# Optimization experiments

Hardware: AMD Instinct MI355X
Metric: run time of the kernel (lower is better)

Reference implementation:

```python
import jax, jax.numpy as jnp
import numpy as np

N_NODES = 100000
N_EDGES = 1600000
N_GRAPHS = 256
F_IN = 54


def setup_inputs() -> dict:
    key = jax.random.key(0)
    ks = jax.random.split(key, 16)
    x = jax.random.normal(ks[0], (N_NODES, F_IN), dtype=jnp.float32)
    edge_index = jax.random.randint(ks[1], (2, N_EDGES), 0, N_NODES, dtype=jnp.int32)
    batch = jnp.sort(jax.random.randint(ks[2], (N_NODES,), 0, N_GRAPHS, dtype=jnp.int32))

    def lin(k, fi, fo):
        kw, kb = jax.random.split(k)
        lim = 1.0 / np.sqrt(fi)
        W = jax.random.uniform(kw, (fi, fo), minval=-lim, maxval=lim, dtype=jnp.float32)
        b = jax.random.uniform(kb, (fo,), minval=-lim, maxval=lim, dtype=jnp.float32)
        return W, b

    W1, b1 = lin(ks[3], 54, 54)
    W2, b2 = lin(ks[4], 54, 108)
    W3, b3 = lin(ks[5], 108, 216)
    Wf1, bf1 = lin(ks[6], 216, 1024)
    Wf2, bf2 = lin(ks[7], 1024, 128)
    return {"x": x, "edge_index": edge_index, "batch": batch,
            "W1": W1, "b1": b1, "W2": W2, "b2": b2, "W3": W3, "b3": b3,
            "Wf1": Wf1, "bf1": bf1, "Wf2": Wf2, "bf2": bf2}


def _gcn_norm(edge_index, n):
    # add self-loops, symmetric degree normalization (PyG GCNConv default)
    loop = jnp.arange(n, dtype=edge_index.dtype)
    row = jnp.concatenate([edge_index[0], loop])
    col = jnp.concatenate([edge_index[1], loop])
    deg = jax.ops.segment_sum(jnp.ones_like(col, dtype=jnp.float32), col, num_segments=n)
    dinv = jnp.where(deg > 0, jax.lax.rsqrt(deg), 0.0)
    norm = dinv[row] * dinv[col]
    return row, col, norm


def _gcn_conv(x, row, col, norm, W, b, n):
    h = x @ W                                  # [N, Fout]
    msg = h[row] * norm[:, None]               # [E+N, Fout] gather + scale
    out = jax.ops.segment_sum(msg, col, num_segments=n)  # scatter-add
    return out + b


def reference(x, edge_index, batch, W1, b1, W2, b2, W3, b3, Wf1, bf1, Wf2, bf2):
    n = x.shape[0]
    row, col, norm = _gcn_norm(edge_index, n)
    h = jax.nn.relu(_gcn_conv(x, row, col, norm, W1, b1, n))
    h = jax.nn.relu(_gcn_conv(h, row, col, norm, W2, b2, n))
    h = jax.nn.relu(_gcn_conv(h, row, col, norm, W3, b3, n))
    # global mean pool per graph
    sums = jax.ops.segment_sum(h, batch, num_segments=N_GRAPHS)
    cnts = jax.ops.segment_sum(jnp.ones((n,), jnp.float32), batch, num_segments=N_GRAPHS)
    pooled = sums / jnp.maximum(cnts, 1.0)[:, None]   # [G, 216]
    g = jax.nn.relu(pooled @ Wf1 + bf1)               # dropout = identity (eval)
    return g @ Wf2 + bf2                              # [G, 128]
```

## Files before the change

### kernel.cpp

```cpp
#include <hip/hip_runtime.h>


typedef _Float16 f16;
typedef _Float16 f16x2 __attribute__((ext_vector_type(2)));
typedef _Float16 f16x8 __attribute__((ext_vector_type(8)));
typedef float f32x4 __attribute__((ext_vector_type(4)));

static __host__ __device__ inline int cdiv(int a, int b) { return (a + b - 1) / b; }

constexpr int BSPAN = 512;
constexpr int EPB   = 4096;
constexpr int EPT   = EPB / 256;

__device__ __forceinline__ void wpack_one(const float* W, f16* Wb, int K, int F,
                                          int KT, int idx) {
    int j = idx & 7;
    int lane = (idx >> 3) & 63;
    int fi = idx >> 9;
    int kt = fi % KT;
    int nt = fi / KT;
    int k = kt * 32 + (lane >> 4) * 8 + j;
    int nn = nt * 16 + (lane & 15);
    Wb[idx] = (k < K && nn < F) ? (f16)W[k * F + nn] : (f16)0.f;
}

__global__ __launch_bounds__(256) void k_init(
        const int* __restrict__ batch, int* __restrict__ start,
        float* __restrict__ psum, int* __restrict__ bktCnt, int* __restrict__ bktCur,
        const int* __restrict__ col,
        const float* __restrict__ W1, const float* __restrict__ W2,
        const float* __restrict__ W3, f16* __restrict__ w1b,
        f16* __restrict__ w2b, f16* __restrict__ w3b,
        int e, int nb, int n, int g) {
    __shared__ int hist[256];
    int t = threadIdx.x;
    int i = blockIdx.x * blockDim.x + t;
    hist[t] = 0;
    __syncthreads();
    int ebase = blockIdx.x * EPB;
#pragma unroll
    for (int j = 0; j < EPT; j++) {
        int idx = ebase + j * 256 + t;
        if (idx < e) atomicAdd(&hist[col[idx] >> 9], 1);
    }
    if (i < g * 216) psum[i] = 0.f;
    if (i < 256) bktCur[i] = 0;
    constexpr int T1 = 4 * 2 * 512;
    constexpr int T2 = 7 * 2 * 512;
    constexpr int T3 = 14 * 4 * 512;
    if (i < T1) wpack_one(W1, w1b, 54, 54, 2, i);
    else if (i < T1 + T2) wpack_one(W2, w2b, 54, 108, 2, i - T1);
    else if (i < T1 + T2 + T3) wpack_one(W3, w3b, 108, 216, 4, i - T1 - T2);
    if (i < n) {
        int b = batch[i];
        int bp = (i == 0) ? -1 : batch[i - 1];
        for (int gg = bp + 1; gg <= b; gg++) start[gg] = i;
        if (i == n - 1)
            for (int gg = b + 1; gg <= g; gg++) start[gg] = n;
    }
    __syncthreads();
    if (t < nb && hist[t] > 0) atomicAdd(&bktCnt[t], hist[t]);
}

__device__ __forceinline__ int scan256_ex(int* sbuf, int v, int t) {
    sbuf[t] = v;
    __syncthreads();
    for (int off = 1; off < 256; off <<= 1) {
        int x = sbuf[t];
        int y = (t >= off) ? sbuf[t - off] : 0;
        __syncthreads();
        sbuf[t] = x + y;
        __syncthreads();
    }
    return sbuf[t] - v;
}

__global__ __launch_bounds__(256) void k_bkt_part(const int* __restrict__ row,
                                                  const int* __restrict__ col,
                                                  const int* __restrict__ bktCnt,
                                                  int* bktCur, unsigned int* __restrict__ ebuf,
                                                  int e, int nb) {
    __shared__ int sbuf[256];
    __shared__ int hist[256];
    __shared__ int base[256];
    __shared__ int lcur[256];
    int t = threadIdx.x;
    int boff = scan256_ex(sbuf, (t < nb) ? bktCnt[t] : 0, t);
    hist[t] = 0; lcur[t] = 0;
    __syncthreads();
    int bs = blockIdx.x * EPB;
    unsigned int pk[EPT];
    int b[EPT];
#pragma unroll
    for (int j = 0; j < EPT; j++) {
        int idx = bs + j * 256 + t;
        if (idx < e) {
            int c = col[idx];
            pk[j] = ((unsigned int)(c & (BSPAN - 1)) << 17) | (unsigned int)row[idx];
            b[j] = c >> 9;
            atomicAdd(&hist[b[j]], 1);
        } else b[j] = -1;
    }
    __syncthreads();
    if (t < nb && hist[t] > 0) base[t] = boff + atomicAdd(&bktCur[t], hist[t]);
    __syncthreads();
#pragma unroll
    for (int j = 0; j < EPT; j++) {
        if (b[j] >= 0) {
            int lofs = atomicAdd(&lcur[b[j]], 1);
            ebuf[base[b[j]] + lofs] = pk[j];
        }
    }
}

__global__ __launch_bounds__(256) void k_bkt_build(const unsigned int* __restrict__ ebuf,
                                                   const int* __restrict__ bktCnt,
                                                   int* __restrict__ rowptr,
                                                   float* __restrict__ dinv,
                                                   int* __restrict__ eSrc,
                                                   int n, int nb) {
    __shared__ int sbuf[256];
    __shared__ int hist[BSPAN];
    __shared__ int cur[BSPAN];
    int t = threadIdx.x;
    int bkt = blockIdx.x;

    int boff_ex = scan256_ex(sbuf, (t < nb) ? bktCnt[t] : 0, t);
    __shared__ int boff_s, cnt_s;
    if (t == bkt) boff_s = boff_ex;
    if (t == 0) cnt_s = bktCnt[bkt];
    hist[t] = 0; hist[t + 256] = 0;
    __syncthreads();
    int es = boff_s, ee = boff_s + cnt_s;

    {
        int i = es + t;
        for (; i + 3 * 256 < ee; i += 4 * 256) {
            unsigned p0 = ebuf[i], p1 = ebuf[i + 256], p2 = ebuf[i + 512], p3 = ebuf[i + 768];
            atomicAdd(&hist[p0 >> 17], 1);
            atomicAdd(&hist[p1 >> 17], 1);
            atomicAdd(&hist[p2 >> 17], 1);
            atomicAdd(&hist[p3 >> 17], 1);
        }
        for (; i < ee; i += 256) atomicAdd(&hist[ebuf[i] >> 17], 1);
    }
    __syncthreads();

    int h0 = hist[2 * t], h1 = hist[2 * t + 1];
    __syncthreads();
    int ex = scan256_ex(sbuf, h0 + h1, t);
    int e0 = es + ex, e1 = e0 + h0;

    int node0 = bkt * BSPAN;
    int n0 = node0 + 2 * t, n1 = node0 + 2 * t + 1;
    if (n0 <= n) rowptr[n0] = e0;
    if (n1 <= n) rowptr[n1] = e1;
    if (n0 < n) dinv[n0] = rsqrtf((float)(h0 + 1));
    if (n1 < n) dinv[n1] = rsqrtf((float)(h1 + 1));
    cur[2 * t] = e0; cur[2 * t + 1] = e1;
    __syncthreads();

    {
        int i = es + t;
        for (; i + 3 * 256 < ee; i += 4 * 256) {
            unsigned p0 = ebuf[i], p1 = ebuf[i + 256], p2 = ebuf[i + 512], p3 = ebuf[i + 768];
            int s0 = atomicAdd(&cur[p0 >> 17], 1);
            int s1 = atomicAdd(&cur[p1 >> 17], 1);
            int s2 = atomicAdd(&cur[p2 >> 17], 1);
            int s3 = atomicAdd(&cur[p3 >> 17], 1);
            eSrc[s0] = (int)(p0 & 0x1FFFFu);
            eSrc[s1] = (int)(p1 & 0x1FFFFu);
            eSrc[s2] = (int)(p2 & 0x1FFFFu);
            eSrc[s3] = (int)(p3 & 0x1FFFFu);
        }
        for (; i < ee; i += 256) {
            unsigned int p = ebuf[i];
            int slot = atomicAdd(&cur[p >> 17], 1);
            eSrc[slot] = (int)(p & 0x1FFFFu);
        }
    }
}

template <int F, int RS>
__global__ void k_prescale(const float* __restrict__ x, const float* __restrict__ dinv,
                           f16* __restrict__ xs, int n) {
    constexpr int CH = F / 2;
    int idx = blockIdx.x * blockDim.x + threadIdx.x;
    if (idx >= n * CH) return;
    int node = idx / CH;
    int c = idx - node * CH;
    float d = dinv[node];
    float2 v = *reinterpret_cast<const float2*>(x + (long long)node * F + c * 2);
    f16x2 h;
    h[0] = (f16)(v.x * d);
    h[1] = (f16)(v.y * d);
    *reinterpret_cast<f16x2*>(xs + (long long)node * RS + c * 2) = h;
}

template <int F, int RS>
__global__ __launch_bounds__(256) void k_gatherw(
        const int* __restrict__ rowptr, const int* __restrict__ eSrc,
        const float* __restrict__ dinv, const f16* __restrict__ hs,
        f16* __restrict__ out, int n) {
    constexpr int CGN = RS / 8;
    constexpr int EPW = 64 / CGN;
    int wave = threadIdx.x >> 6;
    int lane = threadIdx.x & 63;
    int eslot = lane / CGN;
    int cg = lane & (CGN - 1);
    int node = blockIdx.x * 4 + wave;
    if (node >= n) return;
    int ch0 = cg * 8;
    int lim = F - ch0;
    if (lim > 8) lim = 8;
    if (lim < 0) lim = 0;

    int rs_ = rowptr[node], re = rowptr[node + 1];
    float di = dinv[node];
    int deg = re - rs_;
    int myidx = 0;
    if (lane < deg) myidx = eSrc[rs_ + lane];

    const f16x8* src = reinterpret_cast<const f16x8*>(hs);
    float acc[8];
#pragma unroll
    for (int j = 0; j < 8; j++) acc[j] = 0.f;

    if (eslot == 0) {
        f16x8 v = src[(long long)node * CGN + cg];
#pragma unroll
        for (int j = 0; j < 8; j++) acc[j] += (float)v[j];
    }

    int nfull = deg < 64 ? deg : 64;
    for (int base = 0; base < nfull; base += 8 * EPW) {
        int sidx[8];
#pragma unroll
        for (int u = 0; u < 8; u++) {
            int idx = base + u * EPW + eslot;
            sidx[u] = __shfl(myidx, idx < 63 ? idx : 63);
        }
        f16x8 v[8];
#pragma unroll
        for (int u = 0; u < 8; u++) {
            int idx = base + u * EPW + eslot;
            if (idx < nfull) v[u] = src[(long long)sidx[u] * CGN + cg];
        }
#pragma unroll
        for (int u = 0; u < 8; u++) {
            int idx = base + u * EPW + eslot;
            if (idx < nfull) {
#pragma unroll
                for (int j = 0; j < 8; j++) acc[j] += (float)v[u][j];
            }
        }
    }
    for (int e = rs_ + 64 + eslot; e < re; e += EPW) {
        int s = eSrc[e];
        f16x8 v = src[(long long)s * CGN + cg];
#pragma unroll
        for (int j = 0; j < 8; j++) acc[j] += (float)v[j];
    }

#pragma unroll
    for (int j = 0; j < 8; j++)
        if (j >= lim) acc[j] = 0.f;
#pragma unroll
    for (int m = CGN; m < 64; m <<= 1)
#pragma unroll
        for (int j = 0; j < 8; j++) acc[j] += __shfl_xor(acc[j], m);

    if (eslot == 0) {
        f16x8 o;
#pragma unroll
        for (int j = 0; j < 8; j++) o[j] = (f16)(acc[j] * di);
        *reinterpret_cast<f16x8*>(out + (long long)node * RS + ch0) = o;
    }
}

template <int F, int KTILES, int NTILES, int FOUT, int OSTR>
__global__ __launch_bounds__(256) void k_gcn_fused(
        const int* __restrict__ rowptr, const int* __restrict__ eSrc,
        const float* __restrict__ dinv, const f16* __restrict__ hs,
        const f16* __restrict__ Wb, const float* __restrict__ bias,
        f16* __restrict__ outh, int n) {
    constexpr int KPAD = KTILES * 32;
    constexpr int KP   = KPAD + 8;
    constexpr int CGN  = KPAD / 8;
    constexpr int EPH  = 32 / CGN;

    __shared__ __align__(16) f16 a_lds[64 * KP];

    int t = threadIdx.x;
    int node0 = blockIdx.x * 64;
    int w = t >> 6;
    int lane = t & 63;
    int half = lane >> 5;
    int l = lane & 31;
    int eslot = l / CGN;
    int cg = l & (CGN - 1);
    int ch0 = cg * 8;
    int lim = F - ch0;
    if (lim > 8) lim = 8;
    if (lim < 0) lim = 0;
    int lbase = half * 32;

    const f16x8* src = reinterpret_cast<const f16x8*>(hs);
    int nodeBase = node0 + w * 16;

    for (int i = 0; i < 8; i++) {
        int node = nodeBase + 2 * i + half;
        float acc[8];
#pragma unroll
        for (int j = 0; j < 8; j++) acc[j] = 0.f;
        float di = 0.f;

        if (node < n) {
            int rs_ = rowptr[node], re = rowptr[node + 1];
            di = dinv[node];
            int deg = re - rs_;
            int myidx = 0;
            if (l < deg) myidx = eSrc[rs_ + l];

            if (eslot == 0) {
                f16x8 v = src[(long long)node * CGN + cg];
#pragma unroll
                for (int j = 0; j < 8; j++) acc[j] += (float)v[j];
            }

            int nfull = deg < 32 ? deg : 32;
            if (nfull > 0) {
                int sidx[8];
#pragma unroll
                for (int u = 0; u < 8; u++) {
                    int idx = u * EPH + eslot;
                    sidx[u] = __shfl(myidx, lbase + (idx < 31 ? idx : 31));
                }
                f16x8 v[8];
#pragma unroll
                for (int u = 0; u < 8; u++) {
                    int idx = u * EPH + eslot;
                    if (idx < nfull) v[u] = src[(long long)sidx[u] * CGN + cg];
                }
#pragma unroll
                for (int u = 0; u < 8; u++) {
                    int idx = u * EPH + eslot;
                    if (idx < nfull) {
#pragma unroll
                        for (int j = 0; j < 8; j++) acc[j] += (float)v[u][j];
                    }
                }
            }
            for (int e = rs_ + 32 + eslot; e < re; e += EPH) {
                int s = eSrc[e];
                f16x8 v = src[(long long)s * CGN + cg];
#pragma unroll
                for (int j = 0; j < 8; j++) acc[j] += (float)v[j];
            }

#pragma unroll
            for (int j = 0; j < 8; j++)
                if (j >= lim) acc[j] = 0.f;
#pragma unroll
            for (int m = CGN; m < 32; m <<= 1)
#pragma unroll
                for (int j = 0; j < 8; j++) acc[j] += __shfl_xor(acc[j], m);
        }

        if (eslot == 0) {
            f16x8 o;
#pragma unroll
            for (int j = 0; j < 8; j++) o[j] = (f16)(acc[j] * di);
            *reinterpret_cast<f16x8*>(&a_lds[(w * 16 + 2 * i + half) * KP + ch0]) = o;
        }
    }
    __syncthreads();

    int quad = lane >> 4;
    int col = lane & 15;

    f16x8 afr[KTILES];
#pragma unroll
    for (int kt = 0; kt < KTILES; kt++)
        afr[kt] = *reinterpret_cast<const f16x8*>(
            &a_lds[(16 * w + col) * KP + kt * 32 + quad * 8]);

    int nodeC = node0 + 16 * w + quad * 4;
    float dv[4];
#pragma unroll
    for (int r = 0; r < 4; r++) {
        int nd = nodeC + r;
        dv[r] = (nd < n) ? dinv[nd] : 0.f;
    }

    const f16x8* wb = reinterpret_cast<const f16x8*>(Wb);
#pragma unroll
    for (int nt = 0; nt < NTILES; nt++) {
        f16x8 bfr[KTILES];
#pragma unroll
        for (int kt = 0; kt < KTILES; kt++)
            bfr[kt] = wb[(nt * KTILES + kt) * 64 + lane];
        f32x4 acc = {0.f, 0.f, 0.f, 0.f};
#pragma unroll
        for (int kt = 0; kt < KTILES; kt++)
            acc = __builtin_amdgcn_mfma_f32_16x16x32_f16(afr[kt], bfr[kt], acc, 0, 0, 0);

        int ch = nt * 16 + col;
        if (ch < FOUT) {
            float bval = bias[ch];
#pragma unroll
            for (int r = 0; r < 4; r++) {
                int nd = nodeC + r;
                if (nd < n)
                    outh[(long long)nd * OSTR + ch] =
                        (f16)(fmaxf(acc[r] + bval, 0.f) * dv[r]);
            }
        }
    }
}

template <int KTILES, int NTILES, int K, int FOUT>
__global__ __launch_bounds__(256) void k_gemm_pool(
        const f16* __restrict__ in, const f16* __restrict__ Wb,
        const float* __restrict__ bias, const int* __restrict__ batch,
        float* __restrict__ psum, int n) {
    constexpr int KPAD = KTILES * 32;
    constexpr int KP   = KPAD + 8;
    constexpr int V8   = KPAD / 8;
    constexpr int NSLOT = 4;

    __shared__ f16 a_lds[64 * KP];
    __shared__ float psum_l[NSLOT * FOUT];

    int t = threadIdx.x;
    int node0 = blockIdx.x * 64;

    const f16x8* inp = reinterpret_cast<const f16x8*>(in);
    for (int f = t; f < 64 * V8; f += 256) {
        int node = f / V8;
        int v = f - node * V8;
        f16x8 val = {};
        if (node0 + node < n) val = inp[(long long)(node0 + node) * V8 + v];
        *reinterpret_cast<f16x8*>(&a_lds[node * KP + v * 8]) = val;
    }
    for (int i = t; i < NSLOT * FOUT; i += 256) psum_l[i] = 0.f;
    __syncthreads();

    int w = t >> 6;
    int lane = t & 63;
    int quad = lane >> 4;
    int col = lane & 15;

    f16x8 afr[KTILES];
#pragma unroll
    for (int kt = 0; kt < KTILES; kt++)
        afr[kt] = *reinterpret_cast<const f16x8*>(
            &a_lds[(16 * w + col) * KP + kt * 32 + quad * 8]);

    int nodeC = node0 + 16 * w + quad * 4;
    int gb[4];
#pragma unroll
    for (int r = 0; r < 4; r++) {
        int nd = nodeC + r;
        gb[r] = (nd < n) ? batch[nd] : -1;
    }
    int g0 = batch[node0];

    const f16x8* wb = reinterpret_cast<const f16x8*>(Wb);
#pragma unroll
    for (int nt = 0; nt < NTILES; nt++) {
        f16x8 bfr[KTILES];
#pragma unroll
        for (int kt = 0; kt < KTILES; kt++)
            bfr[kt] = wb[(nt * KTILES + kt) * 64 + lane];
        f32x4 acc = {0.f, 0.f, 0.f, 0.f};
#pragma unroll
        for (int kt = 0; kt < KTILES; kt++)
            acc = __builtin_amdgcn_mfma_f32_16x16x32_f16(afr[kt], bfr[kt], acc, 0, 0, 0);

        int ch = nt * 16 + col;
        if (ch < FOUT) {
            float bval = bias[ch];
            if (gb[0] == gb[3] && gb[0] >= 0) {
                float s = fmaxf(acc[0] + bval, 0.f) + fmaxf(acc[1] + bval, 0.f)
                        + fmaxf(acc[2] + bval, 0.f) + fmaxf(acc[3] + bval, 0.f);
                int slot = gb[0] - g0;
                if (slot < NSLOT) atomicAdd(&psum_l[slot * FOUT + ch], s);
                else atomicAdd(&psum[gb[0] * FOUT + ch], s);
            } else {
#pragma unroll
                for (int r = 0; r < 4; r++) {
                    if (gb[r] < 0) continue;
                    float v = fmaxf(acc[r] + bval, 0.f);
                    int slot = gb[r] - g0;
                    if (slot < NSLOT) atomicAdd(&psum_l[slot * FOUT + ch], v);
                    else atomicAdd(&psum[gb[r] * FOUT + ch], v);
                }
            }
        }
    }

    __syncthreads();
    int lastNode = node0 + 63;
    if (lastNode >= n) lastNode = n - 1;
    int nsl = batch[lastNode] - g0 + 1;
    if (nsl > NSLOT) nsl = NSLOT;
    for (int f = t; f < nsl * FOUT; f += 256) {
        float v = psum_l[f];
        if (v != 0.f) atomicAdd(&psum[(g0 + f / FOUT) * FOUT + (f % FOUT)], v);
    }
}

__global__ void k_fc1(const float* __restrict__ P, const int* __restrict__ start,
                      const float* __restrict__ W, const float* __restrict__ bias,
                      float* __restrict__ out) {
    int row = blockIdx.x >> 2;
    int o = (blockIdx.x & 3) * 256 + threadIdx.x;
    int cnt = start[row + 1] - start[row];
    float scale = 1.0f / fmaxf((float)cnt, 1.0f);
    __shared__ float prow[216];
    if (threadIdx.x < 216) prow[threadIdx.x] = P[row * 216 + threadIdx.x] * scale;
    __syncthreads();
    float acc = bias[o];
    for (int k = 0; k < 216; k++) acc += prow[k] * W[k * 1024 + o];
    out[row * 1024 + o] = fmaxf(acc, 0.f);
}
__global__ void k_fc2(const float* __restrict__ G, const float* __restrict__ W,
                      const float* __restrict__ bias, float* __restrict__ out) {
    int row = blockIdx.x;
    int o = threadIdx.x;
    __shared__ float grow[1024];
    for (int k = threadIdx.x; k < 1024; k += 128) grow[k] = G[row * 1024 + k];
    __syncthreads();
    float acc = bias[o];
    for (int k = 0; k < 1024; k++) acc += grow[k] * W[k * 128 + o];
    out[row * 128 + o] = acc;
}

extern "C" void kernel_launch(void* const* d_in, const int* in_sizes, int n_in,
                              void* d_out, int out_size, void* d_ws, size_t ws_size,
                              hipStream_t stream) {
    const float* x     = (const float*)d_in[0];
    const int*   ei    = (const int*)d_in[1];
    const int*   batch = (const int*)d_in[2];
    const float* W1  = (const float*)d_in[3];
    const float* b1  = (const float*)d_in[4];
    const float* W2  = (const float*)d_in[5];
    const float* b2  = (const float*)d_in[6];
    const float* W3  = (const float*)d_in[7];
    const float* b3  = (const float*)d_in[8];
    const float* Wf1 = (const float*)d_in[9];
    const float* bf1 = (const float*)d_in[10];
    const float* Wf2 = (const float*)d_in[11];
    const float* bf2 = (const float*)d_in[12];
    float* out = (float*)d_out;

    const int N = in_sizes[0] / 54;
    const int E = in_sizes[1] / 2;
    const int G = 256;
    const int* row = ei;
    const int* col = ei + E;
    const int NB = cdiv(N, BSPAN);
    const int NBLK_A = cdiv(E, EPB);

    char* ws = (char*)d_ws;
    size_t off = 0;
    auto carve = [&](size_t bytes) {
        void* p = ws + off;
        off += (bytes + 255) & ~(size_t)255;
        return p;
    };
    int*   rowptr  = (int*)carve((size_t)(N + 1) * 4);
    int*   bktCnt  = (int*)carve(256 * 4);
    int*   bktCur  = (int*)carve(256 * 4);
    int*   eSrc    = (int*)carve((size_t)E * 4);
    float* dinv    = (float*)carve((size_t)N * 4);
    f16*   xs      = (f16*)carve((size_t)N * 64 * 2);
    f16*   hsbuf   = (f16*)carve((size_t)N * 128 * 2);
    f16*   bufA    = (f16*)carve((size_t)N * 128 * 2);
    unsigned int* ebuf = (unsigned int*)carve((size_t)E * 4);
    float* psum    = (float*)carve((size_t)G * 216 * 4);
    float* gbuf    = (float*)carve((size_t)G * 1024 * 4);
    int*   start   = (int*)carve((size_t)(G + 1) * 4);
    f16*   w1b     = (f16*)carve((size_t)4 * 2 * 512 * 2);
    f16*   w2b     = (f16*)carve((size_t)7 * 2 * 512 * 2);
    f16*   w3b     = (f16*)carve((size_t)14 * 4 * 512 * 2);

    const int T = 256;
    hipMemsetAsync(bktCnt, 0, 256 * 4, stream);

    int gInit = cdiv(N, T) > NBLK_A ? cdiv(N, T) : NBLK_A;
    k_init<<<gInit, T, 0, stream>>>(batch, start, psum, bktCnt, bktCur, col,
                                    W1, W2, W3, w1b, w2b, w3b, E, NB, N, G);

    k_bkt_part<<<NBLK_A, 256, 0, stream>>>(row, col, bktCnt, bktCur, ebuf, E, NB);
    k_bkt_build<<<NB, 256, 0, stream>>>(ebuf, bktCnt, rowptr, dinv, eSrc, N, NB);

    k_prescale<54, 64><<<cdiv(N * 27, T), T, 0, stream>>>(x, dinv, xs, N);

    const int GB = cdiv(N, 64);

    k_gcn_fused<54, 2, 4, 54, 64><<<GB, 256, 0, stream>>>(
        rowptr, eSrc, dinv, xs, w1b, b1, hsbuf, N);

    k_gcn_fused<54, 2, 7, 108, 128><<<GB, 256, 0, stream>>>(
        rowptr, eSrc, dinv, hsbuf, w2b, b2, bufA, N);

    k_gatherw<108, 128><<<cdiv(N, 4), 256, 0, stream>>>(rowptr, eSrc, dinv, bufA, hsbuf, N);
    k_gemm_pool<4, 14, 108, 216><<<GB, 256, 0, stream>>>(
        hsbuf, w3b, b3, batch, psum, N);

    k_fc1<<<G * 4, T, 0, stream>>>(psum, start, Wf1, bf1, gbuf);
    k_fc2<<<G, 128, 0, stream>>>(gbuf, Wf2, bf2, out);
}
```

Measured before the change: 379.6 us.

## Prefetch next node's row pointers and neighbor indices in GCN aggregation loop

Loads all 17 rowptr entries and 16 dinv values for the warp's nodes once up front and distributes them by shuffle, replacing per-node scalar loads. Software-pipelines the per-node loop so the next node's edge-index load and self-feature load are issued while the current node's neighbor gathers are in flight. This hides the dependent rowptr->eSrc->feature latency chain, at the cost of extra registers that may lower occupancy.

```diff
diff --git a/kernel.cpp b/kernel.cpp
--- a/kernel.cpp
+++ b/kernel.cpp
@@ -308,71 +308,89 @@
     const f16x8* src = reinterpret_cast<const f16x8*>(hs);
     int nodeBase = node0 + w * 16;
 
+    int rpIdx = nodeBase + (lane < 17 ? lane : 16);
+    if (rpIdx > n) rpIdx = n;
+    int rp = rowptr[rpIdx];
+    int dvIdx = nodeBase + (lane < 16 ? lane : 15);
+    if (dvIdx > n - 1) dvIdx = n - 1;
+    float dvl = dinv[dvIdx];
+
+    int rs_c = __shfl(rp, half);
+    int re_c = __shfl(rp, 1 + half);
+    int deg_c = re_c - rs_c;
+    int my_c = 0;
+    if (l < deg_c) my_c = eSrc[rs_c + l];
+    f16x8 sv_c = {};
+    if (eslot == 0 && nodeBase + half < n)
+        sv_c = src[(long long)(nodeBase + half) * CGN + cg];
+
     for (int i = 0; i < 8; i++) {
         int node = nodeBase + 2 * i + half;
+        int nfull = deg_c < 32 ? deg_c : 32;
+
+        int sidx[8];
+#pragma unroll
+        for (int u = 0; u < 8; u++) {
+            int idx = u * EPH + eslot;
+            sidx[u] = __shfl(my_c, lbase + (idx < 31 ? idx : 31));
+        }
+        f16x8 v[8];
+#pragma unroll
+        for (int u = 0; u < 8; u++) {
+            int idx = u * EPH + eslot;
+            if (idx < nfull) v[u] = src[(long long)sidx[u] * CGN + cg];
+        }
+
+        int rs_n = 0, re_n = 0, deg_n = 0, my_n = 0;
+        f16x8 sv_n = {};
+        if (i < 7) {
+            rs_n = __shfl(rp, 2 * i + 2 + half);
+            re_n = __shfl(rp, 2 * i + 3 + half);
+            deg_n = re_n - rs_n;
+            if (l < deg_n) my_n = eSrc[rs_n + l];
+            int node2 = nodeBase + 2 * i + 2 + half;
+            if (eslot == 0 && node2 < n)
+                sv_n = src[(long long)node2 * CGN + cg];
+        }
+
         float acc[8];
 #pragma unroll
         for (int j = 0; j < 8; j++) acc[j] = 0.f;
-        float di = 0.f;
-
-        if (node < n) {
-            int rs_ = rowptr[node], re = rowptr[node + 1];
-            di = dinv[node];
-            int deg = re - rs_;
-            int myidx = 0;
-            if (l < deg) myidx = eSrc[rs_ + l];
-
-            if (eslot == 0) {
-                f16x8 v = src[(long long)node * CGN + cg];
-#pragma unroll
-                for (int j = 0; j < 8; j++) acc[j] += (float)v[j];
+        if (eslot == 0) {
+#pragma unroll
+            for (int j = 0; j < 8; j++) acc[j] += (float)sv_c[j];
+        }
+#pragma unroll
+        for (int u = 0; u < 8; u++) {
+            int idx = u * EPH + eslot;
+            if (idx < nfull) {
+#pragma unroll
+                for (int j = 0; j < 8; j++) acc[j] += (float)v[u][j];
             }
-
-            int nfull = deg < 32 ? deg : 32;
-            if (nfull > 0) {
-                int sidx[8];
-#pragma unroll
-                for (int u = 0; u < 8; u++) {
-                    int idx = u * EPH + eslot;
-                    sidx[u] = __shfl(myidx, lbase + (idx < 31 ? idx : 31));
-                }
-                f16x8 v[8];
-#pragma unroll
-                for (int u = 0; u < 8; u++) {
-                    int idx = u * EPH + eslot;
-                    if (idx < nfull) v[u] = src[(long long)sidx[u] * CGN + cg];
-                }
-#pragma unroll
-                for (int u = 0; u < 8; u++) {
-                    int idx = u * EPH + eslot;
-                    if (idx < nfull) {
-#pragma unroll
-                        for (int j = 0; j < 8; j++) acc[j] += (float)v[u][j];
-                    }
-                }
-            }
-            for (int e = rs_ + 32 + eslot; e < re; e += EPH) {
-                int s = eSrc[e];
-                f16x8 v = src[(long long)s * CGN + cg];
-#pragma unroll
-                for (int j = 0; j < 8; j++) acc[j] += (float)v[j];
-            }
-
-#pragma unroll
-            for (int j = 0; j < 8; j++)
-                if (j >= lim) acc[j] = 0.f;
-#pragma unroll
-            for (int m = CGN; m < 32; m <<= 1)
-#pragma unroll
-                for (int j = 0; j < 8; j++) acc[j] += __shfl_xor(acc[j], m);
-        }
-
+        }
+        for (int e = rs_c + 32 + eslot; e < re_c; e += EPH) {
+            int s = eSrc[e];
+            f16x8 vv = src[(long long)s * CGN + cg];
+#pragma unroll
+            for (int j = 0; j < 8; j++) acc[j] += (float)vv[j];
+        }
+
+#pragma unroll
+        for (int j = 0; j < 8; j++)
+            if (j >= lim) acc[j] = 0.f;
+#pragma unroll
+        for (int m = CGN; m < 32; m <<= 1)
+#pragma unroll
+            for (int j = 0; j < 8; j++) acc[j] += __shfl_xor(acc[j], m);
+
+        float di = (node < n) ? __shfl(dvl, 2 * i + half) : 0.f;
         if (eslot == 0) {
             f16x8 o;
 #pragma unroll
             for (int j = 0; j < 8; j++) o[j] = (f16)(acc[j] * di);
             *reinterpret_cast<f16x8*>(&a_lds[(w * 16 + 2 * i + half) * KP + ch0]) = o;
         }
+        rs_c = rs_n; re_c = re_n; deg_c = deg_n; my_c = my_n; sv_c = sv_n;
     }
     __syncthreads();
 
```

Measured after the change: 361.5 us (median of 3 runs). 1.05x faster.
